# Kernel tuning notes

Measured on AMD Instinct MI355X. Metric: run time of the kernel, lower is better.

Reference implementation:

```python
import jax, jax.numpy as jnp
import numpy as np

B, N, T, F, H, HEADS, E, EDIM, P = 4, 1000, 8, 64, 64, 4, 16000, 16, 5
NEG_SLOPE = 0.2


def _seg_softmax(e, seg, n):
    # segment softmax over destination nodes; every segment is nonempty (self-loops)
    m = jax.ops.segment_max(e, seg, num_segments=n)
    ex = jnp.exp(e - m[seg])
    s = jax.ops.segment_sum(ex, seg, num_segments=n)
    return ex / s[seg]


def _gat(x, ei, W, a_src, a_dst, b):
    # PyG GATConv with concat=False (mean over heads), self-loops already in ei
    n = x.shape[0]
    heads, hh = a_src.shape
    h = (x @ W).reshape(n, heads, hh)                       # [N, heads, H]
    asrc = (h * a_src).sum(-1)                              # [N, heads]
    adst = (h * a_dst).sum(-1)
    src, dst = ei[0], ei[1]
    e = jax.nn.leaky_relu(asrc[src] + adst[dst], NEG_SLOPE)  # [E2, heads]
    alpha = _seg_softmax(e, dst, n)
    out = jax.ops.segment_sum(alpha[:, :, None] * h[src], dst, num_segments=n)
    return out.mean(1) + b                                   # [N, H]


def _gru_cell(x, h, Wih, Whh, bih, bhh):
    gi = x @ Wih.T + bih
    gh = h @ Whh.T + bhh
    i_r, i_z, i_n = jnp.split(gi, 3, axis=-1)
    h_r, h_z, h_n = jnp.split(gh, 3, axis=-1)
    r = jax.nn.sigmoid(i_r + h_r)
    z = jax.nn.sigmoid(i_z + h_z)
    nn_ = jnp.tanh(i_n + r * h_n)
    return (1.0 - z) * nn_ + z * h


def setup_inputs() -> dict:
    key = jax.random.key(0)
    ks = jax.random.split(key, 20)
    rn = lambda k, shp, s: (jax.random.normal(k, shp, jnp.float32) * s)
    inp = {}
    inp['x'] = jax.random.normal(ks[0], (B, N, T, F), jnp.float32)
    inp['edge_index_seq'] = jax.random.randint(ks[1], (B, T, 2, E), 0, N)
    inp['edge_feat_seq'] = jax.random.normal(ks[2], (B, T, E, EDIM), jnp.float32)
    inp['W1'] = rn(ks[3], (F, HEADS * H), 1 / np.sqrt(F))
    inp['att_src1'] = rn(ks[4], (HEADS, H), 1 / np.sqrt(H))
    inp['att_dst1'] = rn(ks[5], (HEADS, H), 1 / np.sqrt(H))
    inp['b1'] = jnp.zeros((H,), jnp.float32)
    inp['W2'] = rn(ks[6], (H, HEADS * H), 1 / np.sqrt(H))
    inp['att_src2'] = rn(ks[7], (HEADS, H), 1 / np.sqrt(H))
    inp['att_dst2'] = rn(ks[8], (HEADS, H), 1 / np.sqrt(H))
    inp['b2'] = jnp.zeros((H,), jnp.float32)
    inp['edge_W'] = rn(ks[9], (EDIM, H), 1 / np.sqrt(EDIM))
    inp['edge_b'] = jnp.zeros((H,), jnp.float32)
    inp['Wih0'] = rn(ks[10], (3 * H, H), 1 / np.sqrt(H))
    inp['Whh0'] = rn(ks[11], (3 * H, H), 1 / np.sqrt(H))
    inp['bih0'] = jnp.zeros((3 * H,), jnp.float32)
    inp['bhh0'] = jnp.zeros((3 * H,), jnp.float32)
    inp['Wih1'] = rn(ks[12], (3 * H, H), 1 / np.sqrt(H))
    inp['Whh1'] = rn(ks[13], (3 * H, H), 1 / np.sqrt(H))
    inp['bih1'] = jnp.zeros((3 * H,), jnp.float32)
    inp['bhh1'] = jnp.zeros((3 * H,), jnp.float32)
    inp['pW1'] = rn(ks[14], (H, H), 1 / np.sqrt(H))
    inp['pb1'] = jnp.zeros((H,), jnp.float32)
    inp['pW2'] = rn(ks[15], (H, 2 * P), 1 / np.sqrt(H))
    inp['pb2'] = jnp.zeros((2 * P,), jnp.float32)
    return inp


def reference(x, edge_index_seq, edge_feat_seq, W1, att_src1, att_dst1, b1,
              W2, att_src2, att_dst2, b2, edge_W, edge_b,
              Wih0, Whh0, bih0, bhh0, Wih1, Whh1, bih1, bhh1,
              pW1, pb1, pW2, pb2):
    Bs, Ns, Ts, Fs = x.shape
    G = Bs * Ts
    # [B,N,T,F] -> [B*T, N, F] (graph per (b,t))
    xg = x.transpose(0, 2, 1, 3).reshape(G, Ns, Fs)
    ei = edge_index_seq.reshape(G, 2, -1)
    # add self-loops (PyG GATConv default)
    sl = jnp.broadcast_to(jnp.arange(Ns), (G, 2, Ns))
    ei = jnp.concatenate([ei, sl], axis=-1)

    def per_graph(xt, e):
        h = jax.nn.relu(_gat(xt, e, W1, att_src1, att_dst1, b1))
        return _gat(h, e, W2, att_src2, att_dst2, b2)

    h = jax.vmap(per_graph)(xg, ei)                         # [G, N, H]
    Hd = h.shape[-1]
    # note: original computes edge_embedding(edge_feat) but never uses it (dead code)
    h = h.reshape(Bs, Ts, Ns, Hd).transpose(0, 2, 1, 3).reshape(Bs * Ns, Ts, Hd)
    xs = h.transpose(1, 0, 2)                               # [T, B*N, H]
    h0 = jnp.zeros((Bs * Ns, Hd), x.dtype)

    def step(carry, xt):
        h1, h2 = carry
        h1n = _gru_cell(xt, h1, Wih0, Whh0, bih0, bhh0)
        h2n = _gru_cell(h1n, h2, Wih1, Whh1, bih1, bhh1)
        return (h1n, h2n), None

    (_, hT), _ = jax.lax.scan(step, (h0, h0), xs)           # hT: [B*N, H]
    mid = jax.nn.relu(hT @ pW1 + pb1)
    pred = mid @ pW2 + pb2                                  # [B*N, 2P]
    return pred.reshape(Bs, Ns, P, 2)
```

## Files before the change

### kernel.cpp

```cpp
#include <hip/hip_runtime.h>
#include <math.h>

#define BB 4
#define NN 1000
#define TT 8
#define FF 64
#define HH 64
#define NHEADS 4
#define EE 16000
#define E2 17000
#define GG (BB*TT)
#define GN (GG*NN)
#define NROWS (BB*NN)

__device__ __forceinline__ float sigmoidf_(float x) {
    return 1.f / (1.f + __expf(-x));
}
__device__ __forceinline__ float tanhf_(float x) {
    x = fminf(fmaxf(x, -15.f), 15.f);
    float e = __expf(2.f * x);
    return (e - 1.f) / (e + 1.f);
}
__device__ __forceinline__ float leaky_(float x) {
    return (x > 0.f) ? x : 0.2f * x;
}

__global__ void count_edges(const int* __restrict__ ei, int* __restrict__ counts) {
    int g = blockIdx.y;
    int e = blockIdx.x * 256 + threadIdx.x;
    if (e >= E2) return;
    int dst;
    if (e < EE) dst = ei[(size_t)g * 2 * EE + EE + e];
    else        dst = e - EE;
    atomicAdd(&counts[g * NN + dst], 1);
}

__global__ __launch_bounds__(256) void scan_offsets_pg(const int* __restrict__ counts,
                                                       int* __restrict__ offs) {
    __shared__ int tot[256];
    int g = blockIdx.x;
    int tid = threadIdx.x;
    int base = tid * 4;
    int c0 = 0, c1 = 0, c2 = 0, c3 = 0;
    if (base < NN) {
        int4 v = *(const int4*)(counts + (size_t)g * NN + base);
        c0 = v.x; c1 = v.y; c2 = v.z; c3 = v.w;
    }
    int s = c0 + c1 + c2 + c3;
    tot[tid] = s;
    __syncthreads();
    for (int off = 1; off < 256; off <<= 1) {
        int y = (tid >= off) ? tot[tid - off] : 0;
        __syncthreads();
        tot[tid] += y;
        __syncthreads();
    }
    int run = g * E2 + tot[tid] - s;
    if (base < NN) {
        int4 o;
        o.x = run; run += c0;
        o.y = run; run += c1;
        o.z = run; run += c2;
        o.w = run;
        *(int4*)(offs + (size_t)g * NN + base) = o;
    }
    if (g == 0 && tid == 0) offs[GN] = GG * E2;
}

__global__ void scatter_edges(const int* __restrict__ ei, const int* __restrict__ offs,
                              int* __restrict__ cursor, int* __restrict__ csr) {
    int g = blockIdx.y;
    int e = blockIdx.x * 256 + threadIdx.x;
    if (e >= E2) return;
    int src, dst;
    if (e < EE) {
        src = ei[(size_t)g * 2 * EE + e];
        dst = ei[(size_t)g * 2 * EE + EE + e];
    } else {
        src = dst = e - EE;
    }
    int i = g * NN + dst;
    int pos = offs[i] + atomicAdd(&cursor[i], 1);
    csr[pos] = src;
}

#define PIN64_(arr)                                        \
    _Pragma("unroll")                                      \
    for (int _pi = 0; _pi < 64; ++_pi)                     \
        asm volatile("" : "+v"((arr)[_pi]));

template <int MODE>
__global__ __launch_bounds__(256) void gat_linear(
    const float* __restrict__ in, const float* __restrict__ W,
    const float* __restrict__ att_s, const float* __restrict__ att_d,
    float* __restrict__ hlin, float* __restrict__ asrc, float* __restrict__ adst) {
    const int ROWS = 10;
    const int CH = NN / ROWS;
    int g = blockIdx.x / CH;
    int n0 = (blockIdx.x % CH) * ROWS;
    int tid = threadIdx.x;
    float wcol[FF];
#pragma unroll
    for (int f = 0; f < FF; ++f) wcol[f] = W[f * 256 + tid];
    int head = tid >> 6, lane = tid & 63;
    float as = att_s[head * HH + lane];
    float ad = att_d[head * HH + lane];
    int b = g / TT, t = g % TT;
    for (int r = 0; r < ROWS; ++r) {
        int n = n0 + r;
        const float* xrow;
        if (MODE == 0) xrow = in + (((size_t)(b * NN + n) * TT + t) * FF);
        else           xrow = in + ((size_t)(g * NN + n) * FF);
        float acc = 0.f;
#pragma unroll
        for (int f = 0; f < FF; ++f) acc = fmaf(xrow[f], wcol[f], acc);
        hlin[((size_t)(g * NN + n) << 8) + (lane << 2) + head] = acc;
        float s1 = acc * as, s2 = acc * ad;
#pragma unroll
        for (int off = 32; off; off >>= 1) {
            s1 += __shfl_xor(s1, off, 64);
            s2 += __shfl_xor(s2, off, 64);
        }
        if (lane == 0) {
            asrc[(size_t)(g * NN + n) * NHEADS + head] = s1;
            adst[(size_t)(g * NN + n) * NHEADS + head] = s2;
        }
    }
}

__global__ __launch_bounds__(256) void gat_edge(
    const float* __restrict__ hlin, const float* __restrict__ asrc,
    const float* __restrict__ adst, const int* __restrict__ offs,
    const int* __restrict__ csr, const float* __restrict__ bias,
    float* __restrict__ out, int do_relu) {
    __shared__ float pbuf[4][64][4];
    __shared__ int   sbuf[4][64];
    __shared__ int   degs[4];
    int tid = threadIdx.x;
    int lane = tid & 63, w = tid >> 6;
    int B = blockIdx.x;
    int x = B & 7, j = B >> 3;
    int graph = x + 8 * (j / 250);
    int node = graph * NN + ((j % 250) << 2) + w;
    int beg = offs[node], end = offs[node + 1];
    int deg = end - beg;
    if (lane == 0) degs[w] = deg;
    __syncthreads();
    int maxdeg = max(max(degs[0], degs[1]), max(degs[2], degs[3]));
    int nchunk = (maxdeg + 63) >> 6;

    float4 ad = *(const float4*)(adst + (size_t)node * 4);
    const float* asrc_g = asrc + (size_t)graph * NN * 4;
    const float* hg = hlin + ((size_t)graph * NN << 8);

    float4 acc = make_float4(0.f, 0.f, 0.f, 0.f);
    float4 ssum = make_float4(0.f, 0.f, 0.f, 0.f);
    for (int c = 0; c < nchunk; ++c) {
        int e0 = beg + (c << 6);
        int myedge = e0 + lane;
        float4 p = make_float4(0.f, 0.f, 0.f, 0.f);
        int src = 0;
        if (myedge < end) {
            src = csr[myedge];
            float4 a = *(const float4*)(asrc_g + (size_t)src * 4);
            p.x = __expf(leaky_(a.x + ad.x));
            p.y = __expf(leaky_(a.y + ad.y));
            p.z = __expf(leaky_(a.z + ad.z));
            p.w = __expf(leaky_(a.w + ad.w));
        }
        float4 t = p;
#pragma unroll
        for (int off = 1; off < 64; off <<= 1) {
            t.x += __shfl_xor(t.x, off, 64);
            t.y += __shfl_xor(t.y, off, 64);
            t.z += __shfl_xor(t.z, off, 64);
            t.w += __shfl_xor(t.w, off, 64);
        }
        ssum.x += t.x; ssum.y += t.y; ssum.z += t.z; ssum.w += t.w;
        *(float4*)&pbuf[w][lane][0] = p;
        sbuf[w][lane] = src;
        __syncthreads();
        int cnt = end - e0;
        if (cnt > 64) cnt = 64;
        int cnt8 = (cnt + 7) & ~7;
        for (int e = 0; e < cnt8; e += 8) {
            float4 p0 = *(const float4*)&pbuf[w][e + 0][0];
            float4 p1 = *(const float4*)&pbuf[w][e + 1][0];
            float4 p2 = *(const float4*)&pbuf[w][e + 2][0];
            float4 p3 = *(const float4*)&pbuf[w][e + 3][0];
            float4 p4 = *(const float4*)&pbuf[w][e + 4][0];
            float4 p5 = *(const float4*)&pbuf[w][e + 5][0];
            float4 p6 = *(const float4*)&pbuf[w][e + 6][0];
            float4 p7 = *(const float4*)&pbuf[w][e + 7][0];
            int s0 = sbuf[w][e + 0], s1 = sbuf[w][e + 1];
            int s2 = sbuf[w][e + 2], s3 = sbuf[w][e + 3];
            int s4 = sbuf[w][e + 4], s5 = sbuf[w][e + 5];
            int s6 = sbuf[w][e + 6], s7 = sbuf[w][e + 7];
            int lo = lane << 2;
            float4 h0 = *(const float4*)(hg + (((size_t)s0) << 8) + lo);
            float4 h1 = *(const float4*)(hg + (((size_t)s1) << 8) + lo);
            float4 h2 = *(const float4*)(hg + (((size_t)s2) << 8) + lo);
            float4 h3 = *(const float4*)(hg + (((size_t)s3) << 8) + lo);
            float4 h4 = *(const float4*)(hg + (((size_t)s4) << 8) + lo);
            float4 h5 = *(const float4*)(hg + (((size_t)s5) << 8) + lo);
            float4 h6 = *(const float4*)(hg + (((size_t)s6) << 8) + lo);
            float4 h7 = *(const float4*)(hg + (((size_t)s7) << 8) + lo);
            acc.x = fmaf(p0.x, h0.x, acc.x); acc.y = fmaf(p0.y, h0.y, acc.y);
            acc.z = fmaf(p0.z, h0.z, acc.z); acc.w = fmaf(p0.w, h0.w, acc.w);
            acc.x = fmaf(p1.x, h1.x, acc.x); acc.y = fmaf(p1.y, h1.y, acc.y);
            acc.z = fmaf(p1.z, h1.z, acc.z); acc.w = fmaf(p1.w, h1.w, acc.w);
            acc.x = fmaf(p2.x, h2.x, acc.x); acc.y = fmaf(p2.y, h2.y, acc.y);
            acc.z = fmaf(p2.z, h2.z, acc.z); acc.w = fmaf(p2.w, h2.w, acc.w);
            acc.x = fmaf(p3.x, h3.x, acc.x); acc.y = fmaf(p3.y, h3.y, acc.y);
            acc.z = fmaf(p3.z, h3.z, acc.z); acc.w = fmaf(p3.w, h3.w, acc.w);
            acc.x = fmaf(p4.x, h4.x, acc.x); acc.y = fmaf(p4.y, h4.y, acc.y);
            acc.z = fmaf(p4.z, h4.z, acc.z); acc.w = fmaf(p4.w, h4.w, acc.w);
            acc.x = fmaf(p5.x, h5.x, acc.x); acc.y = fmaf(p5.y, h5.y, acc.y);
            acc.z = fmaf(p5.z, h5.z, acc.z); acc.w = fmaf(p5.w, h5.w, acc.w);
            acc.x = fmaf(p6.x, h6.x, acc.x); acc.y = fmaf(p6.y, h6.y, acc.y);
            acc.z = fmaf(p6.z, h6.z, acc.z); acc.w = fmaf(p6.w, h6.w, acc.w);
            acc.x = fmaf(p7.x, h7.x, acc.x); acc.y = fmaf(p7.y, h7.y, acc.y);
            acc.z = fmaf(p7.z, h7.z, acc.z); acc.w = fmaf(p7.w, h7.w, acc.w);
        }
        __syncthreads();
    }
    float o = 0.25f * (acc.x / ssum.x + acc.y / ssum.y + acc.z / ssum.z + acc.w / ssum.w)
            + bias[lane];
    if (do_relu) o = fmaxf(o, 0.f);
    out[((size_t)node << 6) + lane] = o;
}

template <int MODE>
__global__ __launch_bounds__(192, 4) void gru_gi(
    const float* __restrict__ in, const float* __restrict__ Wih,
    const float* __restrict__ bih, float* __restrict__ giseq) {
    const int ROWS = 10;
    int j = threadIdx.x;
    float wrow[64];
#pragma unroll
    for (int f4 = 0; f4 < 16; ++f4) {
        float4 w = *(const float4*)(Wih + (size_t)j * 64 + f4 * 4);
        wrow[4 * f4 + 0] = w.x; wrow[4 * f4 + 1] = w.y;
        wrow[4 * f4 + 2] = w.z; wrow[4 * f4 + 3] = w.w;
    }
    PIN64_(wrow)
    float bj = bih[j];
    int q0 = blockIdx.x * ROWS;
    int t = q0 / NROWS;
    int r0 = q0 - t * NROWS;
    for (int rr = 0; rr < ROWS; rr += 2) {
        const float *xa, *xb;
        if (MODE == 0) {
            int ra = r0 + rr, rb = ra + 1;
            int ba = ra / NN, na = ra - ba * NN;
            int bb2 = rb / NN, nb = rb - bb2 * NN;
            xa = in + (((size_t)(ba * TT + t) * NN + na) << 6);
            xb = in + (((size_t)(bb2 * TT + t) * NN + nb) << 6);
        } else {
            xa = in + ((size_t)(q0 + rr) << 6);
            xb = xa + 64;
        }
        float acca = bj, accb = bj;
#pragma unroll
        for (int f4 = 0; f4 < 16; ++f4) {
            float4 a4 = *(const float4*)(xa + f4 * 4);
            float4 b4 = *(const float4*)(xb + f4 * 4);
            acca = fmaf(a4.x, wrow[4 * f4 + 0], acca);
            acca = fmaf(a4.y, wrow[4 * f4 + 1], acca);
            acca = fmaf(a4.z, wrow[4 * f4 + 2], acca);
            acca = fmaf(a4.w, wrow[4 * f4 + 3], acca);
            accb = fmaf(b4.x, wrow[4 * f4 + 0], accb);
            accb = fmaf(b4.y, wrow[4 * f4 + 1], accb);
            accb = fmaf(b4.z, wrow[4 * f4 + 2], accb);
            accb = fmaf(b4.w, wrow[4 * f4 + 3], accb);
        }
        giseq[(size_t)(q0 + rr) * 192 + j] = acca;
        giseq[(size_t)(q0 + rr + 1) * 192 + j] = accb;
    }
}

template <int LAYER>
__global__ __launch_bounds__(128) void gru_rec(
    const float* __restrict__ giseq, const float* __restrict__ Whh,
    const float* __restrict__ bhh, float* __restrict__ outseq) {
    __shared__ float hs[8][64];
    int tid = threadIdx.x;
    int ch = tid & 63, w = tid >> 6;
    float wr[64], wz[64], wn[64];
#pragma unroll
    for (int k4 = 0; k4 < 16; ++k4) {
        float4 a = *(const float4*)(Whh + (size_t)ch * 64 + k4 * 4);
        float4 b = *(const float4*)(Whh + (size_t)(64 + ch) * 64 + k4 * 4);
        float4 c = *(const float4*)(Whh + (size_t)(128 + ch) * 64 + k4 * 4);
        wr[4*k4+0] = a.x; wr[4*k4+1] = a.y; wr[4*k4+2] = a.z; wr[4*k4+3] = a.w;
        wz[4*k4+0] = b.x; wz[4*k4+1] = b.y; wz[4*k4+2] = b.z; wz[4*k4+3] = b.w;
        wn[4*k4+0] = c.x; wn[4*k4+1] = c.y; wn[4*k4+2] = c.z; wn[4*k4+3] = c.w;
    }
    float br = bhh[ch], bz = bhh[64 + ch], bn = bhh[128 + ch];
    int row0 = blockIdx.x * 8 + w * 4;
    float hprev[4];
#pragma unroll
    for (int r = 0; r < 4; ++r) { hs[w * 4 + r][ch] = 0.f; hprev[r] = 0.f; }

    for (int t = 0; t < TT; ++t) {
#pragma unroll
        for (int r = 0; r < 4; ++r) {
            int row = row0 + r;
            const float* gp = giseq + ((size_t)(t * NROWS + row)) * 192;
            float gir = gp[ch], giz = gp[64 + ch], gin = gp[128 + ch];
            float ar = br, az = bz, an = bn;
#pragma unroll
            for (int k4 = 0; k4 < 16; ++k4) {
                float4 h4 = *(const float4*)&hs[w * 4 + r][k4 * 4];
                ar = fmaf(h4.x, wr[4*k4+0], ar); ar = fmaf(h4.y, wr[4*k4+1], ar);
                ar = fmaf(h4.z, wr[4*k4+2], ar); ar = fmaf(h4.w, wr[4*k4+3], ar);
                az = fmaf(h4.x, wz[4*k4+0], az); az = fmaf(h4.y, wz[4*k4+1], az);
                az = fmaf(h4.z, wz[4*k4+2], az); az = fmaf(h4.w, wz[4*k4+3], az);
                an = fmaf(h4.x, wn[4*k4+0], an); an = fmaf(h4.y, wn[4*k4+1], an);
                an = fmaf(h4.z, wn[4*k4+2], an); an = fmaf(h4.w, wn[4*k4+3], an);
            }
            float rg = sigmoidf_(gir + ar);
            float zg = sigmoidf_(giz + az);
            float ng = tanhf_(gin + rg * an);
            float hnew = (1.f - zg) * ng + zg * hprev[r];
            hprev[r] = hnew;
            hs[w * 4 + r][ch] = hnew;
            if (LAYER == 0)
                outseq[(((size_t)(t * NROWS + row)) << 6) + ch] = hnew;
        }
    }
    if (LAYER == 1) {
#pragma unroll
        for (int r = 0; r < 4; ++r)
            outseq[(((size_t)(row0 + r)) << 6) + ch] = hprev[r];
    }
}

__global__ __launch_bounds__(64) void mlp_head(
    const float* __restrict__ hT, const float* __restrict__ pW1,
    const float* __restrict__ pb1, const float* __restrict__ pW2,
    const float* __restrict__ pb2, float* __restrict__ out) {
    int r = blockIdx.x, lane = threadIdx.x;
    __shared__ float hrow[64];
    __shared__ float mid[64];
    hrow[lane] = hT[((size_t)r << 6) + lane];
    __syncthreads();
    float acc = pb1[lane];
#pragma unroll
    for (int k = 0; k < 64; ++k) acc = fmaf(hrow[k], pW1[k * 64 + lane], acc);
    mid[lane] = fmaxf(acc, 0.f);
    __syncthreads();
    if (lane < 10) {
        float o = pb2[lane];
#pragma unroll
        for (int k = 0; k < 64; ++k) o = fmaf(mid[k], pW2[k * 10 + lane], o);
        out[(size_t)r * 10 + lane] = o;
    }
}

extern "C" void kernel_launch(void* const* d_in, const int* in_sizes, int n_in,
                              void* d_out, int out_size, void* d_ws, size_t ws_size,
                              hipStream_t stream) {
    (void)in_sizes; (void)n_in; (void)out_size; (void)ws_size;
    const float* x    = (const float*)d_in[0];
    const int*   ei   = (const int*)d_in[1];
    const float* W1   = (const float*)d_in[3];
    const float* as1  = (const float*)d_in[4];
    const float* ad1  = (const float*)d_in[5];
    const float* b1   = (const float*)d_in[6];
    const float* W2   = (const float*)d_in[7];
    const float* as2  = (const float*)d_in[8];
    const float* ad2  = (const float*)d_in[9];
    const float* b2   = (const float*)d_in[10];
    const float* Wih0 = (const float*)d_in[13];
    const float* Whh0 = (const float*)d_in[14];
    const float* bih0 = (const float*)d_in[15];
    const float* bhh0 = (const float*)d_in[16];
    const float* Wih1 = (const float*)d_in[17];
    const float* Whh1 = (const float*)d_in[18];
    const float* bih1 = (const float*)d_in[19];
    const float* bhh1 = (const float*)d_in[20];
    const float* pW1  = (const float*)d_in[21];
    const float* pb1  = (const float*)d_in[22];
    const float* pW2  = (const float*)d_in[23];
    const float* pb2  = (const float*)d_in[24];
    float* out = (float*)d_out;

    char* ws = (char*)d_ws;
    float* hlin  = (float*)(ws + 0);
    float* giseq = hlin;
    float* asrc  = (float*)(ws + 32768000);
    float* hT    = asrc;
    float* adst  = (float*)(ws + 33280000);
    float* gat1  = (float*)(ws + 33792000);
    float* h1seq = gat1;
    float* gat2  = (float*)(ws + 41984000);
    int* counts  = (int*)(ws + 50176000);
    int* cursor  = (int*)(ws + 50304000);
    int* offs    = (int*)(ws + 50432000);
    int* csr     = (int*)(ws + 50560256);

    hipMemsetAsync(counts, 0, 2 * GN * sizeof(int), stream);

    dim3 egrid((E2 + 255) / 256, GG);
    count_edges<<<egrid, 256, 0, stream>>>(ei, counts);
    scan_offsets_pg<<<GG, 256, 0, stream>>>(counts, offs);
    scatter_edges<<<egrid, 256, 0, stream>>>(ei, offs, cursor, csr);

    gat_linear<0><<<GG * 100, 256, 0, stream>>>(x, W1, as1, ad1, hlin, asrc, adst);
    gat_edge<<<GN / 4, 256, 0, stream>>>(hlin, asrc, adst, offs, csr, b1, gat1, 1);
    gat_linear<1><<<GG * 100, 256, 0, stream>>>(gat1, W2, as2, ad2, hlin, asrc, adst);
    gat_edge<<<GN / 4, 256, 0, stream>>>(hlin, asrc, adst, offs, csr, b2, gat2, 0);

    gru_gi<0><<<3200, 192, 0, stream>>>(gat2, Wih0, bih0, giseq);
    gru_rec<0><<<500, 128, 0, stream>>>(giseq, Whh0, bhh0, h1seq);
    gru_gi<1><<<3200, 192, 0, stream>>>(h1seq, Wih1, bih1, giseq);
    gru_rec<1><<<500, 128, 0, stream>>>(giseq, Whh1, bhh1, hT);

    mlp_head<<<NROWS, 64, 0, stream>>>(hT, pW1, pb1, pW2, pb2, out);
}
```

Measured before the change: 433.1 us.

## Register-tile gat_linear: 64 threads each compute 4 columns over 10 rows

Restructures the GAT linear projection so each 64-thread block handles 10 rows, with each thread computing 4 output columns for all rows in registers. Weights are loaded as float4 once per k-step and reused across the 10 rows, and x rows are read as float4. Before, each thread held one weight column and did scalar loads. The attention reductions become 16-lane shuffles, and the column-to-lane mapping is permuted to match hlin's head-interleaved layout. The cost is more registers per thread and fewer threads per block, which may hurt latency hiding.

Result: slower. 809.2 us (+86.8%).

```diff
diff --git a/kernel.cpp b/kernel.cpp
--- a/kernel.cpp
+++ b/kernel.cpp
@@ -90,7 +90,7 @@
         asm volatile("" : "+v"((arr)[_pi]));
 
 template <int MODE>
-__global__ __launch_bounds__(256) void gat_linear(
+__global__ __launch_bounds__(64, 3) void gat_linear(
     const float* __restrict__ in, const float* __restrict__ W,
     const float* __restrict__ att_s, const float* __restrict__ att_d,
     float* __restrict__ hlin, float* __restrict__ asrc, float* __restrict__ adst) {
@@ -98,32 +98,75 @@
     const int CH = NN / ROWS;
     int g = blockIdx.x / CH;
     int n0 = (blockIdx.x % CH) * ROWS;
-    int tid = threadIdx.x;
-    float wcol[FF];
-#pragma unroll
-    for (int f = 0; f < FF; ++f) wcol[f] = W[f * 256 + tid];
-    int head = tid >> 6, lane = tid & 63;
-    float as = att_s[head * HH + lane];
-    float ad = att_d[head * HH + lane];
+    int l = threadIdx.x;
+    int h = l >> 4, m = l & 15;
     int b = g / TT, t = g % TT;
+
+    const float4* W4 = (const float4*)W;
+    float4 as4 = *(const float4*)(att_s + h * 64 + 4 * m);
+    float4 ad4 = *(const float4*)(att_d + h * 64 + 4 * m);
+
+    const float* xr[ROWS];
+#pragma unroll
     for (int r = 0; r < ROWS; ++r) {
         int n = n0 + r;
-        const float* xrow;
-        if (MODE == 0) xrow = in + (((size_t)(b * NN + n) * TT + t) * FF);
-        else           xrow = in + ((size_t)(g * NN + n) * FF);
-        float acc = 0.f;
-#pragma unroll
-        for (int f = 0; f < FF; ++f) acc = fmaf(xrow[f], wcol[f], acc);
-        hlin[((size_t)(g * NN + n) << 8) + (lane << 2) + head] = acc;
-        float s1 = acc * as, s2 = acc * ad;
-#pragma unroll
-        for (int off = 32; off; off >>= 1) {
+        if (MODE == 0) xr[r] = in + (((size_t)(b * NN + n) * TT + t) * FF);
+        else           xr[r] = in + ((size_t)(g * NN + n) * FF);
+    }
+
+    float4 acc[ROWS];
+#pragma unroll
+    for (int r = 0; r < ROWS; ++r) acc[r] = make_float4(0.f, 0.f, 0.f, 0.f);
+
+#pragma unroll
+    for (int f4 = 0; f4 < 16; ++f4) {
+        float4 w0 = W4[(4 * f4 + 0) * 64 + l];
+        float4 w1 = W4[(4 * f4 + 1) * 64 + l];
+        float4 w2 = W4[(4 * f4 + 2) * 64 + l];
+        float4 w3 = W4[(4 * f4 + 3) * 64 + l];
+#pragma unroll
+        for (int r = 0; r < ROWS; ++r) {
+            float4 x4 = *(const float4*)(xr[r] + 4 * f4);
+            acc[r].x = fmaf(x4.x, w0.x, acc[r].x);
+            acc[r].y = fmaf(x4.x, w0.y, acc[r].y);
+            acc[r].z = fmaf(x4.x, w0.z, acc[r].z);
+            acc[r].w = fmaf(x4.x, w0.w, acc[r].w);
+            acc[r].x = fmaf(x4.y, w1.x, acc[r].x);
+            acc[r].y = fmaf(x4.y, w1.y, acc[r].y);
+            acc[r].z = fmaf(x4.y, w1.z, acc[r].z);
+            acc[r].w = fmaf(x4.y, w1.w, acc[r].w);
+            acc[r].x = fmaf(x4.z, w2.x, acc[r].x);
+            acc[r].y = fmaf(x4.z, w2.y, acc[r].y);
+            acc[r].z = fmaf(x4.z, w2.z, acc[r].z);
+            acc[r].w = fmaf(x4.z, w2.w, acc[r].w);
+            acc[r].x = fmaf(x4.w, w3.x, acc[r].x);
+            acc[r].y = fmaf(x4.w, w3.y, acc[r].y);
+            acc[r].z = fmaf(x4.w, w3.z, acc[r].z);
+            acc[r].w = fmaf(x4.w, w3.w, acc[r].w);
+        }
+    }
+
+#pragma unroll
+    for (int r = 0; r < ROWS; ++r) {
+        int node = g * NN + n0 + r;
+        float* hrow = hlin + ((size_t)node << 8);
+        int s0 = 16 * m + h;
+        hrow[s0 + 0]  = acc[r].x;
+        hrow[s0 + 4]  = acc[r].y;
+        hrow[s0 + 8]  = acc[r].z;
+        hrow[s0 + 12] = acc[r].w;
+        float s1 = acc[r].x * as4.x + acc[r].y * as4.y
+                 + acc[r].z * as4.z + acc[r].w * as4.w;
+        float s2 = acc[r].x * ad4.x + acc[r].y * ad4.y
+                 + acc[r].z * ad4.z + acc[r].w * ad4.w;
+#pragma unroll
+        for (int off = 1; off < 16; off <<= 1) {
             s1 += __shfl_xor(s1, off, 64);
             s2 += __shfl_xor(s2, off, 64);
         }
-        if (lane == 0) {
-            asrc[(size_t)(g * NN + n) * NHEADS + head] = s1;
-            adst[(size_t)(g * NN + n) * NHEADS + head] = s2;
+        if (m == 0) {
+            asrc[(size_t)node * NHEADS + h] = s1;
+            adst[(size_t)node * NHEADS + h] = s2;
         }
     }
 }
@@ -407,9 +450,9 @@
     scan_offsets_pg<<<GG, 256, 0, stream>>>(counts, offs);
     scatter_edges<<<egrid, 256, 0, stream>>>(ei, offs, cursor, csr);
 
-    gat_linear<0><<<GG * 100, 256, 0, stream>>>(x, W1, as1, ad1, hlin, asrc, adst);
+    gat_linear<0><<<GG * 100, 64, 0, stream>>>(x, W1, as1, ad1, hlin, asrc, adst);
     gat_edge<<<GN / 4, 256, 0, stream>>>(hlin, asrc, adst, offs, csr, b1, gat1, 1);
-    gat_linear<1><<<GG * 100, 256, 0, stream>>>(gat1, W2, as2, ad2, hlin, asrc, adst);
+    gat_linear<1><<<GG * 100, 64, 0, stream>>>(gat1, W2, as2, ad2, hlin, asrc, adst);
     gat_edge<<<GN / 4, 256, 0, stream>>>(hlin, asrc, adst, offs, csr, b2, gat2, 0);
 
     gru_gi<0><<<3200, 192, 0, stream>>>(gat2, Wih0, bih0, giseq);
```
